# Kernel optimization log

Hardware: AMD Instinct MI355X
Metric: run time of the kernel (lower is better)

## Reference

```python
import jax, jax.numpy as jnp
import numpy as np

H = 2048      # hidden_size
E = 16        # num_experts
I = 512       # moe_intermediate_size
IS = 2048     # shared_expert_intermediate_size
TOP_K = 2
B, S = 1, 2048


def setup_inputs() -> dict:
    key = jax.random.key(0)
    ks = jax.random.split(key, 9)
    std = 0.02
    return {
        "hidden_states": jax.random.normal(ks[0], (B, S, H), dtype=jnp.float32),
        "gate_w": jax.random.normal(ks[1], (E, H), dtype=jnp.float32) * std,
        "w1": jax.random.normal(ks[2], (E, I, H), dtype=jnp.float32) * std,  # gate_proj per expert
        "w2": jax.random.normal(ks[3], (E, H, I), dtype=jnp.float32) * std,  # down_proj per expert
        "w3": jax.random.normal(ks[4], (E, I, H), dtype=jnp.float32) * std,  # up_proj per expert
        "ws_gate": jax.random.normal(ks[5], (IS, H), dtype=jnp.float32) * std,  # shared gate_proj
        "ws_up": jax.random.normal(ks[6], (IS, H), dtype=jnp.float32) * std,    # shared up_proj
        "ws_down": jax.random.normal(ks[7], (H, IS), dtype=jnp.float32) * std,  # shared down_proj
        "shared_gate_w": jax.random.normal(ks[8], (1, H), dtype=jnp.float32) * std,
    }


def reference(hidden_states, gate_w, w1, w2, w3, ws_gate, ws_up, ws_down, shared_gate_w):
    b, s, h = hidden_states.shape
    x = hidden_states.reshape(-1, h)                     # [T, H]
    T = x.shape[0]

    # Router: softmax in fp32, top-k, renormalize (norm_topk_prob=True)
    router_logits = x @ gate_w.T                         # [T, E]
    routing = jax.nn.softmax(router_logits.astype(jnp.float32), axis=-1)
    topw, sel = jax.lax.top_k(routing, TOP_K)            # [T, K]
    topw = topw / jnp.sum(topw, axis=-1, keepdims=True)
    topw = topw.astype(x.dtype)

    # Scatter top-k weights into dense [T, E] combine matrix (torch_moe semantics)
    combine = jnp.zeros((T, E), dtype=x.dtype).at[jnp.arange(T)[:, None], sel].set(topw)

    # Expert SwiGLU MLPs evaluated densely, masked/weighted by combine
    hmid = jax.nn.silu(jnp.einsum('th,eih->tei', x, w1)) * jnp.einsum('th,eih->tei', x, w3)  # [T,E,I]
    hmid = hmid * combine[:, :, None]
    moe_out = jnp.einsum('tei,ehi->th', hmid, w2)        # [T, H]

    # Shared expert with sigmoid gate
    shared = (jax.nn.silu(x @ ws_gate.T) * (x @ ws_up.T)) @ ws_down.T  # [T, H]
    shared = jax.nn.sigmoid(x @ shared_gate_w.T) * shared

    return (moe_out + shared).reshape(b, s, h)
```

## Files before the change

kernel.cpp:

```cpp
#include <hip/hip_runtime.h>
#include <cmath>

#define HDIM 2048
#define NEXP 16
#define IDIM 512
#define ISDIM 2048
#define NTOK 2048
#define MAXT 48
#define ROWSCAP (MAXT * 128)

#define GU_EXP (MAXT * 4)
#define GU_SH ((NTOK / 128) * (ISDIM / 128))
#define DN_SH ((NTOK / 128) * (HDIM / 256))
#define DN_EXP (MAXT * 8)

typedef short bf16x8 __attribute__((ext_vector_type(8)));
typedef float f32x4 __attribute__((ext_vector_type(4)));
typedef unsigned short us;
typedef __attribute__((address_space(1))) const unsigned int* as1p;
typedef __attribute__((address_space(3))) unsigned int* as3p;

__device__ __forceinline__ us f2bf(float f) {
  unsigned int u = __builtin_bit_cast(unsigned int, f);
  u += 0x7FFFu + ((u >> 16) & 1u);
  return (us)(u >> 16);
}
__device__ __forceinline__ float bf2f(us v) {
  return __builtin_bit_cast(float, (unsigned)v << 16);
}

__device__ __forceinline__ void glds16(const void* g, void* l) {
  __builtin_amdgcn_global_load_lds((as1p)(unsigned long long)g,
                                   (as3p)(unsigned int)(unsigned long long)l, 16, 0, 0);
}

__device__ __forceinline__ void stage_cvt(const float* __restrict__ src,
                                          us* __restrict__ dst) {
  const float4* p = (const float4*)src;
  float4 a = p[0], b = p[1];
  unsigned u0 = __builtin_bit_cast(unsigned, a.x) + 0x8000u;
  unsigned u1 = __builtin_bit_cast(unsigned, a.y) + 0x8000u;
  unsigned u2 = __builtin_bit_cast(unsigned, a.z) + 0x8000u;
  unsigned u3 = __builtin_bit_cast(unsigned, a.w) + 0x8000u;
  unsigned u4 = __builtin_bit_cast(unsigned, b.x) + 0x8000u;
  unsigned u5 = __builtin_bit_cast(unsigned, b.y) + 0x8000u;
  unsigned u6 = __builtin_bit_cast(unsigned, b.z) + 0x8000u;
  unsigned u7 = __builtin_bit_cast(unsigned, b.w) + 0x8000u;
  int4 v;
  v.x = __builtin_amdgcn_perm(u1, u0, 0x07060302);
  v.y = __builtin_amdgcn_perm(u3, u2, 0x07060302);
  v.z = __builtin_amdgcn_perm(u5, u4, 0x07060302);
  v.w = __builtin_amdgcn_perm(u7, u6, 0x07060302);
  *(int4*)dst = v;
}

__global__ __launch_bounds__(256) void k_cvt(
    const float* __restrict__ w1, const float* __restrict__ w2,
    const float* __restrict__ w3, const float* __restrict__ wsg,
    const float* __restrict__ wsu, const float* __restrict__ wsd,
    us* __restrict__ w1b, us* __restrict__ w2b, us* __restrict__ w3b,
    us* __restrict__ wsgb, us* __restrict__ wsub, us* __restrict__ wsdb) {
  int b = blockIdx.x;
  const float* src;
  us* dst;
  if (b < 8192) { src = w1; dst = w1b; }
  else if (b < 16384) { src = w2; dst = w2b; b -= 8192; }
  else if (b < 24576) { src = w3; dst = w3b; b -= 16384; }
  else if (b < 26624) { src = wsg; dst = wsgb; b -= 24576; }
  else if (b < 28672) { src = wsu; dst = wsub; b -= 26624; }
  else { src = wsd; dst = wsdb; b -= 28672; }
  size_t off = ((size_t)b * 256 + threadIdx.x) * 8;
  stage_cvt(src + off, dst + off);
}

__global__ __launch_bounds__(256) void k_router(const float* __restrict__ x,
                                                const float* __restrict__ gate_w,
                                                const float* __restrict__ sgw,
                                                us* __restrict__ xb,
                                                int* __restrict__ sel,
                                                float* __restrict__ wnorm,
                                                float* __restrict__ sig,
                                                int* __restrict__ counts) {
  __shared__ float lg[4][17];
  int tid = threadIdx.x, wid = tid >> 6, lane = tid & 63;
  int t = blockIdx.x * 4 + wid;
  const float4* xrow = reinterpret_cast<const float4*>(x + (size_t)t * HDIM);
  float4 xv[8];
#pragma unroll
  for (int s = 0; s < 8; s++) xv[s] = xrow[s * 64 + lane];
  ushort4* xbrow = reinterpret_cast<ushort4*>(xb + (size_t)t * HDIM);
#pragma unroll
  for (int s = 0; s < 8; s++) {
    ushort4 o;
    o.x = f2bf(xv[s].x); o.y = f2bf(xv[s].y); o.z = f2bf(xv[s].z); o.w = f2bf(xv[s].w);
    xbrow[s * 64 + lane] = o;
  }
#pragma unroll 1
  for (int e = 0; e < 17; e++) {
    const float4* gr =
        reinterpret_cast<const float4*>(e < 16 ? gate_w + (size_t)e * HDIM : sgw);
    float acc = 0.f;
#pragma unroll
    for (int s = 0; s < 8; s++) {
      float4 g = gr[s * 64 + lane];
      acc += xv[s].x * g.x + xv[s].y * g.y + xv[s].z * g.z + xv[s].w * g.w;
    }
#pragma unroll
    for (int off = 32; off; off >>= 1) acc += __shfl_xor(acc, off, 64);
    if (lane == 0) lg[wid][e] = acc;
  }
  if (lane == 0) {
    float* L = lg[wid];
    int i1 = 0; float v1 = L[0];
    for (int i = 1; i < NEXP; i++) if (L[i] > v1) { v1 = L[i]; i1 = i; }
    int i2 = (i1 == 0) ? 1 : 0; float v2 = L[i2];
    for (int i = 0; i < NEXP; i++)
      if (i != i1 && i != i2 && L[i] > v2) { v2 = L[i]; i2 = i; }
    float wa = 1.f / (1.f + expf(v2 - v1));
    sel[2 * t] = i1; sel[2 * t + 1] = i2;
    wnorm[2 * t] = wa; wnorm[2 * t + 1] = 1.f - wa;
    sig[t] = 1.f / (1.f + expf(-L[16]));
    atomicAdd(&counts[i1], 1);
    atomicAdd(&counts[i2], 1);
  }
}

__global__ __launch_bounds__(256) void k_scan_scatter(const int* __restrict__ counts,
                                                      const int* __restrict__ sel,
                                                      const float* __restrict__ wnorm,
                                                      int* __restrict__ tile_expert,
                                                      int* __restrict__ row_token,
                                                      int* __restrict__ rowk,
                                                      float* __restrict__ rw) {
  __shared__ int offs_s[NEXP];
  __shared__ int fill_s[NEXP];
  int tid = threadIdx.x;
  for (int r = tid; r < ROWSCAP; r += 256) row_token[r] = -1;
  if (tid < NEXP) fill_s[tid] = 0;
  if (tid == 0) {
    int acc = 0;
    for (int e = 0; e < NEXP; e++) {
      offs_s[e] = acc;
      int nt = (counts[e] + 127) >> 7;
      for (int i = 0; i < nt; i++) tile_expert[(acc >> 7) + i] = e;
      acc += nt << 7;
    }
    for (int m = acc >> 7; m < MAXT; m++) tile_expert[m] = -1;
  }
  __syncthreads();
  for (int t = tid; t < NTOK; t += 256) {
    for (int k = 0; k < 2; k++) {
      int e = sel[2 * t + k];
      int pos = atomicAdd(&fill_s[e], 1);
      int row = offs_s[e] + pos;
      row_token[row] = t;
      rowk[row] = k;
      rw[row] = wnorm[2 * t + k];
    }
  }
}

__global__ __launch_bounds__(512) void k_gu(
    const us* __restrict__ xb, const us* __restrict__ w1b,
    const us* __restrict__ w3b, const us* __restrict__ wsgb,
    const us* __restrict__ wsub, const int* __restrict__ tile_expert,
    const int* __restrict__ row_token, us* __restrict__ hmid,
    us* __restrict__ hs) {
  __shared__ us As[128 * 64];
  __shared__ us Bs[2][128 * 64];
  __shared__ int toks_s[128];
  int bid = blockIdx.x, tid = threadIdx.x;
  int w = tid >> 6, lane = tid & 63;
  const us *bG, *bU;
  us* outp;
  int mt, n0, ostride;
  if (bid < GU_EXP) {
    mt = bid >> 2; int nt = bid & 3;
    int e = tile_expert[mt];
    if (e < 0) return;
    if (tid < 128) {
      int tk = row_token[mt * 128 + tid];
      toks_s[tid] = tk < 0 ? 0 : tk;
    }
    bG = w1b + ((size_t)e * IDIM + nt * 128) * HDIM;
    bU = w3b + ((size_t)e * IDIM + nt * 128) * HDIM;
    outp = hmid; ostride = IDIM; n0 = nt * 128;
  } else {
    int sb = bid - GU_EXP;
    mt = sb >> 4; int nt = sb & 15;
    if (tid < 128) toks_s[tid] = mt * 128 + tid;
    bG = wsgb + (size_t)(nt * 128) * HDIM;
    bU = wsub + (size_t)(nt * 128) * HDIM;
    outp = hs; ostride = ISDIM; n0 = nt * 128;
  }
  __syncthreads();
  int lr = lane >> 3, lc = lane & 7;
  int swz = (lc ^ lr) * 8;
  const us* aSrc0 = xb + (size_t)toks_s[w * 16 + lr] * HDIM + swz;
  const us* aSrc1 = xb + (size_t)toks_s[w * 16 + 8 + lr] * HDIM + swz;
  int mat = w >> 2, sub = w & 3, wm = sub >> 1, wn = sub & 1;
  const us* bSrc = (mat ? bU : bG) + (size_t)(sub * 32 + lr) * HDIM + swz;
  us* bDst = &Bs[mat][sub * 32 * 64];
  int quad = lane >> 4, l16 = lane & 15, sw = l16 & 7;
  f32x4 acc[4][4] = {};
  for (int k0 = 0; k0 < HDIM; k0 += 64) {
    glds16(aSrc0 + k0, As + w * 1024);
    glds16(aSrc1 + k0, As + w * 1024 + 512);
#pragma unroll
    for (int g = 0; g < 4; g++)
      glds16(bSrc + (size_t)(g * 8) * HDIM + k0, bDst + g * 512);
    __syncthreads();
#pragma unroll
    for (int ks = 0; ks < 2; ks++) {
      int cb = (ks * 4 + quad) ^ sw;
      bf16x8 af[4], bf[4];
#pragma unroll
      for (int ms = 0; ms < 4; ms++)
        af[ms] = *(const bf16x8*)&As[((wm * 64 + ms * 16 + l16) * 8 + cb) * 8];
#pragma unroll
      for (int ns = 0; ns < 4; ns++)
        bf[ns] = *(const bf16x8*)&Bs[mat][((wn * 64 + ns * 16 + l16) * 8 + cb) * 8];
#pragma unroll
      for (int ms = 0; ms < 4; ms++)
#pragma unroll
        for (int ns = 0; ns < 4; ns++)
          acc[ms][ns] = __builtin_amdgcn_mfma_f32_16x16x32_bf16(af[ms], bf[ns], acc[ms][ns], 0, 0, 0);
    }
    __syncthreads();
  }
  us* ub = (us*)Bs;
  if (mat == 1) {
#pragma unroll
    for (int ms = 0; ms < 4; ms++)
#pragma unroll
      for (int ns = 0; ns < 4; ns++)
#pragma unroll
        for (int r = 0; r < 4; r++) {
          int row = wm * 64 + ms * 16 + quad * 4 + r;
          int col = wn * 64 + ns * 16 + l16;
          ub[row * 128 + col] = f2bf(acc[ms][ns][r]);
        }
  }
  __syncthreads();
  if (mat == 0) {
#pragma unroll
    for (int ms = 0; ms < 4; ms++)
#pragma unroll
      for (int ns = 0; ns < 4; ns++)
#pragma unroll
        for (int r = 0; r < 4; r++) {
          int row = wm * 64 + ms * 16 + quad * 4 + r;
          int col = wn * 64 + ns * 16 + l16;
          float g = acc[ms][ns][r];
          float u = bf2f(ub[row * 128 + col]);
          float hv = (g / (1.f + __expf(-g))) * u;
          outp[(size_t)(mt * 128 + row) * ostride + n0 + col] = f2bf(hv);
        }
  }
}

__global__ __launch_bounds__(512) void k_down(
    const us* __restrict__ hmid, const us* __restrict__ hs,
    const us* __restrict__ w2b, const us* __restrict__ wsdb,
    const int* __restrict__ tile_expert, const int* __restrict__ row_token,
    const int* __restrict__ rowk, const float* __restrict__ rw,
    const float* __restrict__ sig, us* __restrict__ slab) {
  __shared__ us As[128 * 64];
  __shared__ us Bs[256 * 64];
  __shared__ int idx_s[128];
  __shared__ float wgt_s[128];
  int bid = blockIdx.x, tid = threadIdx.x;
  int w = tid >> 6, lane = tid & 63;
  const us* aBase;
  const us* bBase;
  int K, mt, n0;
  if (bid < DN_SH) {
    mt = bid >> 3; int nt = bid & 7;
    aBase = hs + (size_t)mt * 128 * ISDIM; K = ISDIM;
    bBase = wsdb + (size_t)(nt * 256) * ISDIM;
    n0 = nt * 256;
    if (tid < 128) {
      int t = mt * 128 + tid;
      idx_s[tid] = 2 * NTOK * HDIM + t * HDIM;
      wgt_s[tid] = sig[t];
    }
  } else {
    int sb = bid - DN_SH;
    mt = sb >> 3; int nt = sb & 7;
    int e = tile_expert[mt];
    if (e < 0) return;
    aBase = hmid + (size_t)mt * 128 * IDIM; K = IDIM;
    bBase = w2b + ((size_t)e * HDIM + nt * 256) * IDIM;
    n0 = nt * 256;
    if (tid < 128) {
      int tk = row_token[mt * 128 + tid];
      if (tk < 0) { idx_s[tid] = -1; wgt_s[tid] = 0.f; }
      else {
        idx_s[tid] = (rowk[mt * 128 + tid] * NTOK + tk) * HDIM;
        wgt_s[tid] = rw[mt * 128 + tid];
      }
    }
  }
  __syncthreads();
  int lr = lane >> 3, lc = lane & 7;
  int swz = (lc ^ lr) * 8;
  const us* aSrc0 = aBase + (size_t)(w * 16 + lr) * K + swz;
  const us* aSrc1 = aBase + (size_t)(w * 16 + 8 + lr) * K + swz;
  const us* bSrc = bBase + (size_t)(w * 32 + lr) * K + swz;
  us* bDst = Bs + w * 32 * 64;
  int wmn = w >> 2, wn = w & 3;
  int quad = lane >> 4, l16 = lane & 15, sw = l16 & 7;
  f32x4 acc[4][4] = {};
  for (int k0 = 0; k0 < K; k0 += 64) {
    glds16(aSrc0 + k0, As + w * 1024);
    glds16(aSrc1 + k0, As + w * 1024 + 512);
#pragma unroll
    for (int g = 0; g < 4; g++)
      glds16(bSrc + (size_t)(g * 8) * K + k0, bDst + g * 512);
    __syncthreads();
#pragma unroll
    for (int ks = 0; ks < 2; ks++) {
      int cb = (ks * 4 + quad) ^ sw;
      bf16x8 af[4], bf[4];
#pragma unroll
      for (int ms = 0; ms < 4; ms++)
        af[ms] = *(const bf16x8*)&As[((wmn * 64 + ms * 16 + l16) * 8 + cb) * 8];
#pragma unroll
      for (int ns = 0; ns < 4; ns++)
        bf[ns] = *(const bf16x8*)&Bs[((wn * 64 + ns * 16 + l16) * 8 + cb) * 8];
#pragma unroll
      for (int ms = 0; ms < 4; ms++)
#pragma unroll
        for (int ns = 0; ns < 4; ns++)
          acc[ms][ns] = __builtin_amdgcn_mfma_f32_16x16x32_bf16(af[ms], bf[ns], acc[ms][ns], 0, 0, 0);
    }
    __syncthreads();
  }
#pragma unroll
  for (int ms = 0; ms < 4; ms++)
#pragma unroll
    for (int r = 0; r < 4; r++) {
      int rr = wmn * 64 + ms * 16 + quad * 4 + r;
      int ix = idx_s[rr];
      if (ix >= 0) {
        float wgt = wgt_s[rr];
        us* orow = slab + (size_t)ix + n0 + wn * 64;
#pragma unroll
        for (int ns = 0; ns < 4; ns++)
          orow[ns * 16 + l16] = f2bf(wgt * acc[ms][ns][r]);
      }
    }
}

__global__ __launch_bounds__(256) void k_combine(const us* __restrict__ slab,
                                                 float* __restrict__ out) {
  size_t i = ((size_t)blockIdx.x * 256 + threadIdx.x) * 8;
  bf16x8 a = *(const bf16x8*)(slab + i);
  bf16x8 b = *(const bf16x8*)(slab + (size_t)NTOK * HDIM + i);
  bf16x8 c = *(const bf16x8*)(slab + 2 * (size_t)NTOK * HDIM + i);
  float4 o[2];
#pragma unroll
  for (int j = 0; j < 8; j++)
    ((float*)o)[j] = bf2f((us)a[j]) + bf2f((us)b[j]) + bf2f((us)c[j]);
  *(float4*)(out + i) = o[0];
  *(float4*)(out + i + 4) = o[1];
}

extern "C" void kernel_launch(void* const* d_in, const int* in_sizes, int n_in,
                              void* d_out, int out_size, void* d_ws, size_t ws_size,
                              hipStream_t stream) {
  const float* x = (const float*)d_in[0];
  const float* gate_w = (const float*)d_in[1];
  const float* w1 = (const float*)d_in[2];
  const float* w2 = (const float*)d_in[3];
  const float* w3 = (const float*)d_in[4];
  const float* wsg = (const float*)d_in[5];
  const float* wsu = (const float*)d_in[6];
  const float* wsd = (const float*)d_in[7];
  const float* sgw = (const float*)d_in[8];
  float* out = (float*)d_out;

  us* xb = (us*)d_ws;
  us* hs = xb + (size_t)NTOK * HDIM;
  us* hmid = hs + (size_t)NTOK * ISDIM;
  us* slab = hmid + (size_t)ROWSCAP * IDIM;
  us* w1b = slab + (size_t)3 * NTOK * HDIM;
  us* w3b = w1b + (size_t)NEXP * IDIM * HDIM;
  us* w2b = w3b + (size_t)NEXP * IDIM * HDIM;
  us* wsgb = w2b + (size_t)NEXP * HDIM * IDIM;
  us* wsub = wsgb + (size_t)ISDIM * HDIM;
  us* wsdb = wsub + (size_t)ISDIM * HDIM;
  float* rw = (float*)(wsdb + (size_t)HDIM * ISDIM);
  float* wnorm = rw + ROWSCAP;
  float* sig = wnorm + 2 * NTOK;
  int* sel = (int*)(sig + NTOK);
  int* row_token = sel + 2 * NTOK;
  int* rowk = row_token + ROWSCAP;
  int* counts = rowk + ROWSCAP;
  int* tile_expert = counts + NEXP;

  hipMemsetAsync(counts, 0, NEXP * sizeof(int), stream);
  k_cvt<<<dim3(30720), dim3(256), 0, stream>>>(w1, w2, w3, wsg, wsu, wsd,
                                               w1b, w2b, w3b, wsgb, wsub, wsdb);
  k_router<<<dim3(NTOK / 4), dim3(256), 0, stream>>>(x, gate_w, sgw, xb, sel, wnorm,
                                                     sig, counts);
  k_scan_scatter<<<dim3(1), dim3(256), 0, stream>>>(counts, sel, wnorm, tile_expert,
                                                    row_token, rowk, rw);
  k_gu<<<dim3(GU_EXP + GU_SH), dim3(512), 0, stream>>>(
      xb, w1b, w3b, wsgb, wsub, tile_expert, row_token, hmid, hs);
  k_down<<<dim3(DN_SH + DN_EXP), dim3(512), 0, stream>>>(
      hmid, hs, w2b, wsdb, tile_expert, row_token, rowk, rw, sig, slab);
  k_combine<<<dim3(NTOK * HDIM / 2048), dim3(256), 0, stream>>>(slab, out);
}
```

Measured before the change: 464.0 us.

## Use nontemporal loads/stores, parallelize scatter per expert, unroll router loop

The weight-conversion and combine kernels now use nontemporal loads and stores, which keeps streaming data from polluting the cache. The single-block scan/scatter kernel is replaced by one wavefront per expert that uses ballot/popcount ranks to place tokens deterministically. It only clears the padding rows rather than the whole row buffer. The router expert loop is unrolled by two. These are several small independent tweaks aimed at the bandwidth-bound conversion pass and a serial bottleneck kernel.

```diff
diff --git a/kernel.cpp b/kernel.cpp
--- a/kernel.cpp
+++ b/kernel.cpp
@@ -16,6 +16,7 @@
 
 typedef short bf16x8 __attribute__((ext_vector_type(8)));
 typedef float f32x4 __attribute__((ext_vector_type(4)));
+typedef unsigned int u32x4 __attribute__((ext_vector_type(4)));
 typedef unsigned short us;
 typedef __attribute__((address_space(1))) const unsigned int* as1p;
 typedef __attribute__((address_space(3))) unsigned int* as3p;
@@ -34,18 +35,18 @@
                                    (as3p)(unsigned int)(unsigned long long)l, 16, 0, 0);
 }
 
-__device__ __forceinline__ void stage_cvt(const float* __restrict__ src,
-                                          us* __restrict__ dst) {
-  const float4* p = (const float4*)src;
-  float4 a = p[0], b = p[1];
-  unsigned u0 = __builtin_bit_cast(unsigned, a.x) + 0x8000u;
-  unsigned u1 = __builtin_bit_cast(unsigned, a.y) + 0x8000u;
-  unsigned u2 = __builtin_bit_cast(unsigned, a.z) + 0x8000u;
-  unsigned u3 = __builtin_bit_cast(unsigned, a.w) + 0x8000u;
-  unsigned u4 = __builtin_bit_cast(unsigned, b.x) + 0x8000u;
-  unsigned u5 = __builtin_bit_cast(unsigned, b.y) + 0x8000u;
-  unsigned u6 = __builtin_bit_cast(unsigned, b.z) + 0x8000u;
-  unsigned u7 = __builtin_bit_cast(unsigned, b.w) + 0x8000u;
+__device__ __forceinline__ void cvt8_nt(const unsigned* __restrict__ src,
+                                        us* __restrict__ dst) {
+  u32x4 a = __builtin_nontemporal_load((const u32x4*)src);
+  u32x4 b = __builtin_nontemporal_load((const u32x4*)(src + 4));
+  unsigned u0 = a.x + 0x8000u;
+  unsigned u1 = a.y + 0x8000u;
+  unsigned u2 = a.z + 0x8000u;
+  unsigned u3 = a.w + 0x8000u;
+  unsigned u4 = b.x + 0x8000u;
+  unsigned u5 = b.y + 0x8000u;
+  unsigned u6 = b.z + 0x8000u;
+  unsigned u7 = b.w + 0x8000u;
   int4 v;
   v.x = __builtin_amdgcn_perm(u1, u0, 0x07060302);
   v.y = __builtin_amdgcn_perm(u3, u2, 0x07060302);
@@ -70,7 +71,7 @@
   else if (b < 28672) { src = wsu; dst = wsub; b -= 26624; }
   else { src = wsd; dst = wsdb; b -= 28672; }
   size_t off = ((size_t)b * 256 + threadIdx.x) * 8;
-  stage_cvt(src + off, dst + off);
+  cvt8_nt((const unsigned*)(src + off), dst + off);
 }
 
 __global__ __launch_bounds__(256) void k_router(const float* __restrict__ x,
@@ -95,7 +96,7 @@
     o.x = f2bf(xv[s].x); o.y = f2bf(xv[s].y); o.z = f2bf(xv[s].z); o.w = f2bf(xv[s].w);
     xbrow[s * 64 + lane] = o;
   }
-#pragma unroll 1
+#pragma unroll 2
   for (int e = 0; e < 17; e++) {
     const float4* gr =
         reinterpret_cast<const float4*>(e < 16 ? gate_w + (size_t)e * HDIM : sgw);
@@ -125,38 +126,40 @@
   }
 }
 
-__global__ __launch_bounds__(256) void k_scan_scatter(const int* __restrict__ counts,
-                                                      const int* __restrict__ sel,
-                                                      const float* __restrict__ wnorm,
-                                                      int* __restrict__ tile_expert,
-                                                      int* __restrict__ row_token,
-                                                      int* __restrict__ rowk,
-                                                      float* __restrict__ rw) {
-  __shared__ int offs_s[NEXP];
-  __shared__ int fill_s[NEXP];
-  int tid = threadIdx.x;
-  for (int r = tid; r < ROWSCAP; r += 256) row_token[r] = -1;
-  if (tid < NEXP) fill_s[tid] = 0;
-  if (tid == 0) {
-    int acc = 0;
-    for (int e = 0; e < NEXP; e++) {
-      offs_s[e] = acc;
-      int nt = (counts[e] + 127) >> 7;
-      for (int i = 0; i < nt; i++) tile_expert[(acc >> 7) + i] = e;
-      acc += nt << 7;
-    }
-    for (int m = acc >> 7; m < MAXT; m++) tile_expert[m] = -1;
-  }
-  __syncthreads();
-  for (int t = tid; t < NTOK; t += 256) {
-    for (int k = 0; k < 2; k++) {
-      int e = sel[2 * t + k];
-      int pos = atomicAdd(&fill_s[e], 1);
-      int row = offs_s[e] + pos;
+__global__ __launch_bounds__(64) void k_scatter(const int* __restrict__ counts,
+                                                const int* __restrict__ sel,
+                                                const float* __restrict__ wnorm,
+                                                int* __restrict__ tile_expert,
+                                                int* __restrict__ row_token,
+                                                int* __restrict__ rowk,
+                                                float* __restrict__ rw) {
+  int e = blockIdx.x, lane = threadIdx.x;
+  int base = 0, total = 0, nt_e = 0, cnt_e = 0;
+  for (int i = 0; i < NEXP; i++) {
+    int c = counts[i];
+    int nt = (c + 127) >> 7;
+    if (i == e) { base = total; cnt_e = c; nt_e = nt; }
+    total += nt << 7;
+  }
+  for (int i = lane; i < nt_e; i += 64) tile_expert[(base >> 7) + i] = e;
+  if (e == NEXP - 1)
+    for (int m = (total >> 7) + lane; m < MAXT; m += 64) tile_expert[m] = -1;
+  for (int r = cnt_e + lane; r < nt_e * 128; r += 64) row_token[base + r] = -1;
+  int run = 0;
+  for (int t0 = 0; t0 < NTOK; t0 += 64) {
+    int t = t0 + lane;
+    int s0 = sel[2 * t], s1 = sel[2 * t + 1];
+    int k = (s1 == e) ? 1 : 0;
+    bool m = (s0 == e) || (s1 == e);
+    unsigned long long mask = __ballot(m);
+    int rank = __popcll(mask & ((1ull << lane) - 1ull));
+    if (m) {
+      int row = base + run + rank;
       row_token[row] = t;
       rowk[row] = k;
       rw[row] = wnorm[2 * t + k];
     }
+    run += __popcll(mask);
   }
 }
 
@@ -355,15 +358,18 @@
 __global__ __launch_bounds__(256) void k_combine(const us* __restrict__ slab,
                                                  float* __restrict__ out) {
   size_t i = ((size_t)blockIdx.x * 256 + threadIdx.x) * 8;
-  bf16x8 a = *(const bf16x8*)(slab + i);
-  bf16x8 b = *(const bf16x8*)(slab + (size_t)NTOK * HDIM + i);
-  bf16x8 c = *(const bf16x8*)(slab + 2 * (size_t)NTOK * HDIM + i);
-  float4 o[2];
-#pragma unroll
-  for (int j = 0; j < 8; j++)
-    ((float*)o)[j] = bf2f((us)a[j]) + bf2f((us)b[j]) + bf2f((us)c[j]);
-  *(float4*)(out + i) = o[0];
-  *(float4*)(out + i + 4) = o[1];
+  bf16x8 a = __builtin_nontemporal_load((const bf16x8*)(slab + i));
+  bf16x8 b = __builtin_nontemporal_load((const bf16x8*)(slab + (size_t)NTOK * HDIM + i));
+  bf16x8 c = __builtin_nontemporal_load((const bf16x8*)(slab + 2 * (size_t)NTOK * HDIM + i));
+  f32x4 o0, o1;
+#pragma unroll
+  for (int j = 0; j < 4; j++)
+    o0[j] = bf2f((us)a[j]) + bf2f((us)b[j]) + bf2f((us)c[j]);
+#pragma unroll
+  for (int j = 0; j < 4; j++)
+    o1[j] = bf2f((us)a[4 + j]) + bf2f((us)b[4 + j]) + bf2f((us)c[4 + j]);
+  __builtin_nontemporal_store(o0, (f32x4*)(out + i));
+  __builtin_nontemporal_store(o1, (f32x4*)(out + i + 4));
 }
 
 extern "C" void kernel_launch(void* const* d_in, const int* in_sizes, int n_in,
@@ -404,8 +410,8 @@
                                                w1b, w2b, w3b, wsgb, wsub, wsdb);
   k_router<<<dim3(NTOK / 4), dim3(256), 0, stream>>>(x, gate_w, sgw, xb, sel, wnorm,
                                                      sig, counts);
-  k_scan_scatter<<<dim3(1), dim3(256), 0, stream>>>(counts, sel, wnorm, tile_expert,
-                                                    row_token, rowk, rw);
+  k_scatter<<<dim3(NEXP), dim3(64), 0, stream>>>(counts, sel, wnorm, tile_expert,
+                                                 row_token, rowk, rw);
   k_gu<<<dim3(GU_EXP + GU_SH), dim3(512), 0, stream>>>(
       xb, w1b, w3b, wsgb, wsub, tile_expert, row_token, hmid, hs);
   k_down<<<dim3(DN_SH + DN_EXP), dim3(512), 0, stream>>>(
```

Result: no change. 463.3 us (-0.1%).
